# Performance work log

Measured on AMD Instinct MI355X. Metric: run time of the kernel, lower is better.

The kernel has to match this reference:

```python
import jax, jax.numpy as jnp
import numpy as np


def _conv(x, w, b, stride, pad):
    # x: [N,C,H,W], w: [O,I,kh,kw]
    y = jax.lax.conv_general_dilated(
        x, w, (stride, stride), [(pad, pad), (pad, pad)],
        dimension_numbers=('NCHW', 'OIHW', 'NCHW'))
    return y + b[None, :, None, None]


def _block(x, w1, b1, w2, b2, stride):
    # BasicBlock with BN folded: conv3x3 -> relu -> conv3x3
    h = jax.nn.relu(_conv(x, w1, b1, stride, 1))
    return _conv(h, w2, b2, 1, 1)


def setup_inputs() -> dict:
    key = jax.random.key(0)
    keys = iter(jax.random.split(key, 64))

    def rn(shape):
        fan_in = int(np.prod(shape[1:])) if len(shape) > 1 else shape[0]
        return jax.random.normal(next(keys), shape, jnp.float32) * (1.0 / np.sqrt(fan_in))

    d = {}
    d['inputs'] = jax.random.normal(next(keys), (128, 3, 64, 64), jnp.float32)
    d['probs'] = jax.random.uniform(next(keys), (128, 15), jnp.float32)
    d['seed_w'] = rn((64, 3, 3, 3))
    d['seed_b'] = jnp.zeros((64,), jnp.float32)
    specs = [(64, 64), (64, 128), (128, 256)]  # (cin, cout) per group
    for g, (ci, co) in enumerate(specs):
        d[f'g{g}_ds_w'] = rn((co, ci, 1, 1))
        d[f'g{g}_ds_b'] = jnp.zeros((co,), jnp.float32)
        d[f'g{g}_b0_w1'] = rn((co, ci, 3, 3))
        d[f'g{g}_b0_b1'] = jnp.zeros((co,), jnp.float32)
        d[f'g{g}_b0_w2'] = rn((co, co, 3, 3))
        d[f'g{g}_b0_b2'] = jnp.zeros((co,), jnp.float32)
        d[f'g{g}_r_w1'] = rn((4, co, co, 3, 3))
        d[f'g{g}_r_b1'] = jnp.zeros((4, co), jnp.float32)
        d[f'g{g}_r_w2'] = rn((4, co, co, 3, 3))
        d[f'g{g}_r_b2'] = jnp.zeros((4, co), jnp.float32)
    d['fc_w'] = rn((1000, 256))
    d['fc_b'] = jnp.zeros((1000,), jnp.float32)
    return d


def reference(inputs, probs, seed_w, seed_b,
              g0_ds_w, g0_ds_b, g0_b0_w1, g0_b0_b1, g0_b0_w2, g0_b0_b2,
              g0_r_w1, g0_r_b1, g0_r_w2, g0_r_b2,
              g1_ds_w, g1_ds_b, g1_b0_w1, g1_b0_b1, g1_b0_w2, g1_b0_b2,
              g1_r_w1, g1_r_b1, g1_r_w2, g1_r_b2,
              g2_ds_w, g2_ds_b, g2_b0_w1, g2_b0_b1, g2_b0_w2, g2_b0_b2,
              g2_r_w1, g2_r_b1, g2_r_w2, g2_r_b2,
              fc_w, fc_b):
    # policy[k, n] in {0,1}: hard-threshold of agent probs at 0.5 (forward_real)
    policy = jnp.where(probs < 0.5, 0.0, 1.0).astype(inputs.dtype).T  # [15, B]
    x = jax.nn.relu(_conv(inputs, seed_w, seed_b, 1, 1))
    groups = [
        (g0_ds_w, g0_ds_b, g0_b0_w1, g0_b0_b1, g0_b0_w2, g0_b0_b2, g0_r_w1, g0_r_b1, g0_r_w2, g0_r_b2, 1),
        (g1_ds_w, g1_ds_b, g1_b0_w1, g1_b0_b1, g1_b0_w2, g1_b0_b2, g1_r_w1, g1_r_b1, g1_r_w2, g1_r_b2, 2),
        (g2_ds_w, g2_ds_b, g2_b0_w1, g2_b0_b1, g2_b0_w2, g2_b0_b2, g2_r_w1, g2_r_b1, g2_r_w2, g2_r_b2, 2),
    ]
    idx = 0
    for (ds_w, ds_b, b0_w1, b0_b1, b0_w2, b0_b2, r_w1, r_b1, r_w2, r_b2, s) in groups:
        # first block of the group: strided, with 1x1 downsample residual
        residual = _conv(x, ds_w, ds_b, s, 0)
        fx = _block(x, b0_w1, b0_b1, b0_w2, b0_b2, s)
        m = policy[idx][:, None, None, None]
        idx += 1
        x = m * jax.nn.relu(residual + fx) + (1.0 - m) * residual
        # remaining 4 identity-residual blocks
        for j in range(4):
            residual = x
            fx = _block(x, r_w1[j], r_b1[j], r_w2[j], r_b2[j], 1)
            m = policy[idx][:, None, None, None]
            idx += 1
            x = m * jax.nn.relu(residual + fx) + (1.0 - m) * residual
    pooled = x.mean(axis=(2, 3))  # global average pool [B, 256]
    return pooled @ fc_w.T + fc_b
```

## Files before the change

### kernel.cpp

```cpp
#include <hip/hip_runtime.h>

using bf = unsigned short;
typedef __attribute__((ext_vector_type(8))) short short8v;
typedef __attribute__((ext_vector_type(4))) float f32x4;
typedef __attribute__((ext_vector_type(4))) unsigned int u32x4;
typedef __attribute__((ext_vector_type(2))) unsigned int u32x2;

__device__ __forceinline__ float bf2f(bf u) { return __uint_as_float(((unsigned)u) << 16); }
__device__ __forceinline__ bf f2bf(float f) {
    unsigned x = __float_as_uint(f);
    x += 0x7fffu + ((x >> 16) & 1u);
    return (bf)(x >> 16);
}

__device__ __forceinline__ void gload16(const bf* g, bf* l) {
    __builtin_amdgcn_global_load_lds(
        (const __attribute__((address_space(1))) void*)g,
        (__attribute__((address_space(3))) void*)l, 16, 0, 0);
}

template <int CI, int CC, int RS, int STRIDE, bool RELU, int CMB, int TH, int TW, int W>
__global__ __launch_bounds__(256, 3) void conv_mfma(
    const bf* __restrict__ X, const bf* __restrict__ Wp,
    const float* __restrict__ bias, bf* __restrict__ Y,
    const bf* __restrict__ res, const float* __restrict__ probs,
    const bf* __restrict__ zpage, int kidx, int Co) {
    constexpr int PAD = (RS == 3) ? 1 : 0;
    constexpr int IN_ROWS = (TH - 1) * STRIDE + RS;
    constexpr int IN_COLS = (TW - 1) * STRIDE + RS;
    constexpr int NG = CC / 8;
    constexpr int HIN = W * STRIDE;
    constexpr int RSRS = RS * RS;
    constexpr int NCH = CI / CC;
    constexpr bool DIRECT = (RS == 1);
    constexpr int TG = IN_ROWS * IN_COLS * NG;
    constexpr int NITER = (TG + 255) / 256;
    constexpr int NPX = TH * TW;
    constexpr int NF = NPX / 32;
    constexpr int TPR = W / TW;
    constexpr int KSH = (STRIDE == 2) ? 1 : 0;

    __shared__ bf sX[DIRECT ? 8 : IN_ROWS * IN_COLS * CC];

    const int tid = threadIdx.x;
    const int n = blockIdx.z;
    const int coBase = blockIdx.y << 6;
    const int bx = blockIdx.x;
    const int tr0 = (bx / TPR) * TH;
    const int tc0 = (bx % TPR) * TW;

    bool active = true;
    if (kidx >= 0) active = (probs[n * 15 + kidx] >= 0.5f);
    if (!active) return;

    const int lane = tid & 63;
    const int wid = tid >> 6;
    const int l15 = lane & 15;
    const int lq = lane >> 4;
    const int wm = wid >> 1;
    const int wn = wid & 1;

    f32x4 acc[2][NF] = {};
    int prow[NF], pcol[NF];
#pragma unroll
    for (int nf = 0; nf < NF; ++nf) {
        int p = wn * (NPX / 2) + nf * 16 + l15;
        prow[nf] = p / TW;
        pcol[nf] = p % TW;
    }

    const bf* Xn = X + (size_t)n * HIN * HIN * CI;

    if constexpr (DIRECT) {
#pragma unroll
        for (int ch = 0; ch < NCH; ++ch) {
#pragma unroll
            for (int kk = 0; kk < CC / 32; ++kk) {
                short8v a[2], b[NF];
#pragma unroll
                for (int mf = 0; mf < 2; ++mf) {
                    int co = coBase + wm * 32 + mf * 16 + l15;
                    a[mf] = *reinterpret_cast<const short8v*>(
                        Wp + ((size_t)ch * Co + co) * CC + kk * 32 + lq * 8);
                }
#pragma unroll
                for (int nf = 0; nf < NF; ++nf) {
                    b[nf] = *reinterpret_cast<const short8v*>(
                        Xn + ((size_t)((tr0 + prow[nf]) * STRIDE) * HIN +
                              (tc0 + pcol[nf]) * STRIDE) * CI + ch * CC + kk * 32 + lq * 8);
                }
#pragma unroll
                for (int mf = 0; mf < 2; ++mf)
#pragma unroll
                    for (int nf = 0; nf < NF; ++nf)
                        acc[mf][nf] = __builtin_amdgcn_mfma_f32_16x16x32_bf16(
                            a[mf], b[nf], acc[mf][nf], 0, 0, 0);
            }
        }
    } else {
        for (int ch = 0; ch < NCH; ++ch) {
            if (ch) __syncthreads();
#pragma unroll
            for (int i = 0; i < NITER; ++i) {
                int g = tid + i * 256;
                if (TG % 256 == 0 || g < TG) {
                    int ir = g / (IN_COLS * NG);
                    int rem = g - ir * (IN_COLS * NG);
                    int ic = rem / NG;
                    int gc = rem - ic * NG;
                    int in_r = tr0 * STRIDE - PAD + ir;
                    int in_c = tc0 * STRIDE - PAD + ic;
                    int gsrc = gc ^ ((ic >> KSH) & (NG - 1));
                    const bf* src = zpage;
                    if ((unsigned)in_r < (unsigned)HIN && (unsigned)in_c < (unsigned)HIN)
                        src = Xn + ((size_t)in_r * HIN + in_c) * CI + ch * CC + gsrc * 8;
                    gload16(src, &sX[(size_t)g * 8]);
                }
            }
            __syncthreads();

            if constexpr (CC >= 32) {
#pragma unroll
                for (int j = 0; j < RSRS; ++j) {
                    const int dh = j / RS;
                    const int dw = j % RS;
#pragma unroll
                    for (int kk = 0; kk < CC / 32; ++kk) {
                        short8v a[2], b[NF];
#pragma unroll
                        for (int mf = 0; mf < 2; ++mf) {
                            int co = coBase + wm * 32 + mf * 16 + l15;
                            a[mf] = *reinterpret_cast<const short8v*>(
                                Wp + (((size_t)(ch * RSRS + j) * Co + co) * CC + kk * 32 + lq * 8));
                        }
#pragma unroll
                        for (int nf = 0; nf < NF; ++nf) {
                            int ir = prow[nf] * STRIDE + dh;
                            int ic = pcol[nf] * STRIDE + dw;
                            int gk = (kk * 4 + lq) ^ ((ic >> KSH) & (NG - 1));
                            b[nf] = *reinterpret_cast<const short8v*>(
                                &sX[((ir * IN_COLS + ic) * NG + gk) * 8]);
                        }
#pragma unroll
                        for (int mf = 0; mf < 2; ++mf)
#pragma unroll
                            for (int nf = 0; nf < NF; ++nf)
                                acc[mf][nf] = __builtin_amdgcn_mfma_f32_16x16x32_bf16(
                                    a[mf], b[nf], acc[mf][nf], 0, 0, 0);
                    }
                }
            } else {
#pragma unroll
                for (int kt = 0; kt < 3; ++kt) {
                    int j = kt * 4 + lq;
                    int jj = (j < 9) ? j : 0;
                    int dh = jj / 3, dw = jj % 3;
                    short8v a[2], b[NF];
#pragma unroll
                    for (int mf = 0; mf < 2; ++mf) {
                        int co = coBase + wm * 32 + mf * 16 + l15;
                        a[mf] = *reinterpret_cast<const short8v*>(Wp + ((size_t)j * Co + co) * 8);
                    }
#pragma unroll
                    for (int nf = 0; nf < NF; ++nf) {
                        int ir = prow[nf] + dh;
                        int ic = pcol[nf] + dw;
                        b[nf] = *reinterpret_cast<const short8v*>(&sX[(ir * IN_COLS + ic) * 8]);
                    }
#pragma unroll
                    for (int mf = 0; mf < 2; ++mf)
#pragma unroll
                        for (int nf = 0; nf < NF; ++nf)
                            acc[mf][nf] = __builtin_amdgcn_mfma_f32_16x16x32_bf16(
                                a[mf], b[nf], acc[mf][nf], 0, 0, 0);
                }
            }
        }
    }

#pragma unroll
    for (int mf = 0; mf < 2; ++mf) {
        int co0 = coBase + wm * 32 + mf * 16 + lq * 4;
        float4 b4 = *reinterpret_cast<const float4*>(bias + co0);
        float bb[4] = {b4.x, b4.y, b4.z, b4.w};
#pragma unroll
        for (int nf = 0; nf < NF; ++nf) {
            size_t off = ((size_t)n * W * W + (size_t)(tr0 + prow[nf]) * W + tc0 + pcol[nf]) * Co + co0;
            float v[4];
#pragma unroll
            for (int i = 0; i < 4; ++i) v[i] = acc[mf][nf][i] + bb[i];
            if constexpr (CMB >= 1) {
                u32x2 r2 = *reinterpret_cast<const u32x2*>(res + off);
                bf rr[4] = {(bf)(r2[0] & 0xffff), (bf)(r2[0] >> 16),
                            (bf)(r2[1] & 0xffff), (bf)(r2[1] >> 16)};
#pragma unroll
                for (int i = 0; i < 4; ++i) v[i] = fmaxf(v[i] + bf2f(rr[i]), 0.f);
            }
            if constexpr (RELU) {
#pragma unroll
                for (int i = 0; i < 4; ++i) v[i] = fmaxf(v[i], 0.f);
            }
            unsigned lo = (unsigned)f2bf(v[0]) | ((unsigned)f2bf(v[1]) << 16);
            unsigned hi = (unsigned)f2bf(v[2]) | ((unsigned)f2bf(v[3]) << 16);
            u32x2 o2 = {lo, hi};
            *reinterpret_cast<u32x2*>(Y + off) = o2;
        }
    }
}

#define NSEG 34
struct Seg {
    const float* src;
    bf* dst;
    int Co, Ci, RSRS, CC, JPAD, blk0;
};
struct SegArgs {
    Seg s[NSEG];
};
__global__ void repack_all(SegArgs A) {
    int b = blockIdx.x;
    int lo = 0;
#pragma unroll 1
    for (int i = 1; i < NSEG; ++i)
        if (A.s[i].blk0 <= b) lo = i;
    Seg sg = A.s[lo];
    int NCH_ = (sg.Ci + sg.CC - 1) / sg.CC;
    size_t total8 = ((size_t)NCH_ * sg.JPAD * sg.Co * sg.CC) >> 3;
    size_t i8 = (size_t)(b - sg.blk0) * 256 + threadIdx.x;
    if (i8 >= total8) return;
    size_t e = i8 * 8;
    int cw = (int)(e % sg.CC);
    int co = (int)((e / sg.CC) % sg.Co);
    int j = (int)((e / ((size_t)sg.CC * sg.Co)) % sg.JPAD);
    int ch = (int)(e / ((size_t)sg.CC * sg.Co * sg.JPAD));
    bf tmp[8];
#pragma unroll
    for (int k = 0; k < 8; ++k) {
        int ci = ch * sg.CC + cw + k;
        float v = 0.f;
        if (ci < sg.Ci && j < sg.RSRS) v = sg.src[((size_t)co * sg.Ci + ci) * sg.RSRS + j];
        tmp[k] = f2bf(v);
    }
    u32x4 o;
#pragma unroll
    for (int k = 0; k < 4; ++k) o[k] = (unsigned)tmp[2 * k] | ((unsigned)tmp[2 * k + 1] << 16);
    *reinterpret_cast<u32x4*>(sg.dst + e) = o;
}

__global__ void cvt_in(const float* __restrict__ in, bf* __restrict__ out) {
    size_t idx = (size_t)blockIdx.x * 256 + threadIdx.x;
    int c = (int)(idx & 7);
    size_t pix = idx >> 3;
    int w = (int)(pix & 63);
    int h = (int)((pix >> 6) & 63);
    int n = (int)(pix >> 12);
    float v = 0.f;
    if (c < 3) v = in[(((size_t)n * 3 + c) * 64 + h) * 64 + w];
    out[idx] = f2bf(v);
}

__global__ void zero_k(bf* p) {
    u32x4 z = {0, 0, 0, 0};
    *reinterpret_cast<u32x4*>(p + (size_t)threadIdx.x * 8) = z;
}

__global__ void pool_k(const bf* __restrict__ X, float* __restrict__ pooled) {
    __shared__ float red[8][256];
    int n = blockIdx.x;
    int g = threadIdx.x & 31;
    int slice = threadIdx.x >> 5;
    float acc[8] = {};
    for (int p = slice * 32; p < slice * 32 + 32; ++p) {
        u32x4 v = *reinterpret_cast<const u32x4*>(X + ((size_t)n * 256 + p) * 256 + g * 8);
#pragma unroll
        for (int i = 0; i < 4; ++i) {
            acc[2 * i] += bf2f((bf)(v[i] & 0xffff));
            acc[2 * i + 1] += bf2f((bf)(v[i] >> 16));
        }
    }
#pragma unroll
    for (int i = 0; i < 8; ++i) red[slice][g * 8 + i] = acc[i];
    __syncthreads();
    if (slice == 0) {
#pragma unroll
        for (int i = 0; i < 8; ++i) {
            float s = 0.f;
#pragma unroll
            for (int ss = 0; ss < 8; ++ss) s += red[ss][g * 8 + i];
            pooled[n * 256 + g * 8 + i] = s * (1.f / 256.f);
        }
    }
}

__global__ void fc_k(const float* __restrict__ pooled, const float* __restrict__ fw,
                     const float* __restrict__ fb, float* __restrict__ out) {
    __shared__ float sp[256];
    int n = blockIdx.x;
    sp[threadIdx.x] = pooled[n * 256 + threadIdx.x];
    __syncthreads();
    for (int o = threadIdx.x; o < 1000; o += 256) {
        float acc = fb[o];
        for (int k = 0; k < 256; ++k) acc += sp[k] * fw[(size_t)o * 256 + k];
        out[(size_t)n * 1000 + o] = acc;
    }
}

template <int CIN, int COUT, int S, int TH, int TW, int W, int CC1>
static void run_group(hipStream_t st, bf* X, bf* H, bf* OUT, const bf* zp,
                      bf* wp_ds, const float* ds_b, bf* wp_w1, const float* b1,
                      bf* wp_w2, const float* b2, bf* const* wp_rw1, const float* rb1,
                      bf* const* wp_rw2, const float* rb2, const float* probs_c,
                      int kbase, int NB) {
    dim3 grid((W / TH) * (W / TW), COUT / 64, NB);
    conv_mfma<CIN, 64, 1, S, false, 0, TH, TW, W><<<grid, 256, 0, st>>>(
        X, wp_ds, ds_b, OUT, nullptr, nullptr, zp, -1, COUT);
    conv_mfma<CIN, CC1, 3, S, true, 0, TH, TW, W><<<grid, 256, 0, st>>>(
        X, wp_w1, b1, H, nullptr, probs_c, zp, kbase, COUT);
    conv_mfma<COUT, 64, 3, 1, false, 2, TH, TW, W><<<grid, 256, 0, st>>>(
        H, wp_w2, b2, OUT, OUT, probs_c, zp, kbase, COUT);
    for (int j = 0; j < 4; ++j) {
        conv_mfma<COUT, 64, 3, 1, true, 0, TH, TW, W><<<grid, 256, 0, st>>>(
            OUT, wp_rw1[j], rb1 + j * COUT, H, nullptr, probs_c, zp, kbase + 1 + j, COUT);
        conv_mfma<COUT, 64, 3, 1, false, 2, TH, TW, W><<<grid, 256, 0, st>>>(
            H, wp_rw2[j], rb2 + j * COUT, OUT, OUT, probs_c, zp, kbase + 1 + j, COUT);
    }
}

extern "C" void kernel_launch(void* const* d_in, const int* in_sizes, int n_in,
                              void* d_out, int out_size, void* d_ws, size_t ws_size,
                              hipStream_t stream) {
    (void)in_sizes; (void)n_in; (void)out_size;
    const float* input = (const float*)d_in[0];
    const float* probs = (const float*)d_in[1];
    const float* seed_w = (const float*)d_in[2];
    const float* seed_b = (const float*)d_in[3];
    const float* fc_w = (const float*)d_in[34];
    const float* fc_b = (const float*)d_in[35];

    char* pw = (char*)d_ws;
    auto alloc = [&](size_t bytes) -> void* {
        void* r = (void*)pw;
        pw += ((bytes + 255) & ~(size_t)255);
        return r;
    };

    bf* xin = (bf*)alloc(128ull * 64 * 64 * 8 * 2);
    float* pooled = (float*)alloc(128 * 256 * 4);
    bf* zpage = (bf*)alloc(256);

    SegArgs sa;
    int nseg = 0;
    int blkAcc = 0;
    auto pack = [&](const float* w, int Co_, int Ci_, int RSRS_, int CC_, int JPAD_) -> bf* {
        int NCH_ = (Ci_ + CC_ - 1) / CC_;
        size_t total = (size_t)NCH_ * JPAD_ * Co_ * CC_;
        bf* wp = (bf*)alloc(total * 2);
        sa.s[nseg] = {w, wp, Co_, Ci_, RSRS_, CC_, JPAD_, blkAcc};
        blkAcc += (int)(((total >> 3) + 255) / 256);
        ++nseg;
        return wp;
    };

    zero_k<<<dim3(1), 16, 0, stream>>>(zpage);
    cvt_in<<<dim3(16384), 256, 0, stream>>>(input, xin);

    bf* wpSeed = pack(seed_w, 64, 3, 9, 8, 12);
    const int cis[3] = {64, 64, 128};
    const int cos[3] = {64, 128, 256};
    const int cc1s[3] = {64, 32, 32};
    bf* wp_ds[3];
    bf* wp_w1[3];
    bf* wp_w2[3];
    bf* wp_rw1[3][4];
    bf* wp_rw2[3][4];
    const float *ds_b[3], *b1[3], *b2[3], *rb1[3], *rb2[3];
    for (int g = 0; g < 3; ++g) {
        int base = 4 + g * 10;
        const float* dsw = (const float*)d_in[base + 0];
        ds_b[g] = (const float*)d_in[base + 1];
        const float* w1 = (const float*)d_in[base + 2];
        b1[g] = (const float*)d_in[base + 3];
        const float* w2 = (const float*)d_in[base + 4];
        b2[g] = (const float*)d_in[base + 5];
        const float* rw1 = (const float*)d_in[base + 6];
        rb1[g] = (const float*)d_in[base + 7];
        const float* rw2 = (const float*)d_in[base + 8];
        rb2[g] = (const float*)d_in[base + 9];
        int Ci = cis[g], Co = cos[g];
        wp_ds[g] = pack(dsw, Co, Ci, 1, 64, 1);
        wp_w1[g] = pack(w1, Co, Ci, 9, cc1s[g], 9);
        wp_w2[g] = pack(w2, Co, Co, 9, 64, 9);
        for (int j = 0; j < 4; ++j) {
            wp_rw1[g][j] = pack(rw1 + (size_t)j * Co * Co * 9, Co, Co, 9, 64, 9);
            wp_rw2[g][j] = pack(rw2 + (size_t)j * Co * Co * 9, Co, Co, 9, 64, 9);
        }
    }
    for (int i = nseg; i < NSEG; ++i) sa.s[i] = {nullptr, nullptr, 1, 1, 1, 1, 1, 0x7fffffff};
    repack_all<<<dim3(blkAcc), 256, 0, stream>>>(sa);

    size_t used = (size_t)(pw - (char*)d_ws);
    size_t avail = (ws_size > used) ? (ws_size - used) : 0;
    const size_t PER_IMG = 64ull * 64 * 64 * 2;
    int NB = 128;
    while (NB > 8 && (size_t)3 * NB * PER_IMG + 4096 > avail) NB >>= 1;

    bf* A = (bf*)alloc((size_t)NB * PER_IMG);
    bf* Bb = (bf*)alloc((size_t)NB * PER_IMG);
    bf* C = (bf*)alloc((size_t)NB * PER_IMG);

    for (int n0 = 0; n0 < 128; n0 += NB) {
        const float* pc = probs + (size_t)n0 * 15;
        conv_mfma<8, 8, 3, 1, true, 0, 8, 16, 64><<<dim3(32, 1, NB), 256, 0, stream>>>(
            xin + (size_t)n0 * 64 * 64 * 8, wpSeed, seed_b, A, nullptr, nullptr, zpage, -1, 64);

        run_group<64, 64, 1, 8, 16, 64, 64>(stream, A, Bb, C, zpage,
                                            wp_ds[0], ds_b[0], wp_w1[0], b1[0],
                                            wp_w2[0], b2[0], wp_rw1[0], rb1[0],
                                            wp_rw2[0], rb2[0], pc, 0, NB);
        run_group<64, 128, 2, 8, 16, 32, 32>(stream, C, Bb, A, zpage,
                                             wp_ds[1], ds_b[1], wp_w1[1], b1[1],
                                             wp_w2[1], b2[1], wp_rw1[1], rb1[1],
                                             wp_rw2[1], rb2[1], pc, 5, NB);
        run_group<128, 256, 2, 8, 8, 16, 32>(stream, A, Bb, C, zpage,
                                             wp_ds[2], ds_b[2], wp_w1[2], b1[2],
                                             wp_w2[2], b2[2], wp_rw1[2], rb1[2],
                                             wp_rw2[2], rb2[2], pc, 10, NB);

        pool_k<<<dim3(NB), 256, 0, stream>>>(C, pooled + (size_t)n0 * 256);
    }

    fc_k<<<dim3(128), 256, 0, stream>>>(pooled, fc_w, fc_b, (float*)d_out);
}
```

Before: 2.360 ms.

## Double-buffer conv input tiles and fuse input conversion, zeroing and pool+fc

Adds double-buffered LDS staging to the conv kernel when there are multiple channel chunks and two buffers fit in shared memory. The next chunk's global-to-LDS loads can then be issued while MFMAs run on the current chunk, and one barrier per chunk is removed. The seed conv now reads the fp32 NCHW input directly and converts it in-kernel, which drops the separate cvt_in pass. Zero-page init is folded into repack_all and pool+fc are merged into one kernel. The extra LDS use in double-buffered configs may lower occupancy.

```diff
diff --git a/kernel.cpp b/kernel.cpp
--- a/kernel.cpp
+++ b/kernel.cpp
@@ -19,12 +19,14 @@
         (__attribute__((address_space(3))) void*)l, 16, 0, 0);
 }
 
-template <int CI, int CC, int RS, int STRIDE, bool RELU, int CMB, int TH, int TW, int W>
+template <int CI, int CC, int RS, int STRIDE, bool SEED, bool RELU, int CMB,
+          int TH, int TW, int W>
 __global__ __launch_bounds__(256, 3) void conv_mfma(
-    const bf* __restrict__ X, const bf* __restrict__ Wp,
-    const float* __restrict__ bias, bf* __restrict__ Y,
-    const bf* __restrict__ res, const float* __restrict__ probs,
-    const bf* __restrict__ zpage, int kidx, int Co) {
+    const bf* __restrict__ X, const float* __restrict__ Xf,
+    const bf* __restrict__ Wp, const float* __restrict__ bias,
+    bf* __restrict__ Y, const bf* __restrict__ res,
+    const float* __restrict__ probs, const bf* __restrict__ zpage,
+    int kidx, int Co) {
     constexpr int PAD = (RS == 3) ? 1 : 0;
     constexpr int IN_ROWS = (TH - 1) * STRIDE + RS;
     constexpr int IN_COLS = (TW - 1) * STRIDE + RS;
@@ -39,8 +41,10 @@
     constexpr int NF = NPX / 32;
     constexpr int TPR = W / TW;
     constexpr int KSH = (STRIDE == 2) ? 1 : 0;
-
-    __shared__ bf sX[DIRECT ? 8 : IN_ROWS * IN_COLS * CC];
+    constexpr int HALF = IN_ROWS * IN_COLS * CC;
+    constexpr bool DBUF = (!DIRECT) && (!SEED) && (NCH > 1) && (2 * HALF * 2 <= 65536);
+
+    __shared__ bf sX[DIRECT ? 8 : (DBUF ? 2 * HALF : HALF)];
 
     const int tid = threadIdx.x;
     const int n = blockIdx.z;
@@ -98,27 +102,44 @@
             }
         }
     } else {
-        for (int ch = 0; ch < NCH; ++ch) {
-            if (ch) __syncthreads();
-#pragma unroll
-            for (int i = 0; i < NITER; ++i) {
-                int g = tid + i * 256;
-                if (TG % 256 == 0 || g < TG) {
-                    int ir = g / (IN_COLS * NG);
-                    int rem = g - ir * (IN_COLS * NG);
-                    int ic = rem / NG;
-                    int gc = rem - ic * NG;
-                    int in_r = tr0 * STRIDE - PAD + ir;
-                    int in_c = tc0 * STRIDE - PAD + ic;
-                    int gsrc = gc ^ ((ic >> KSH) & (NG - 1));
-                    const bf* src = zpage;
-                    if ((unsigned)in_r < (unsigned)HIN && (unsigned)in_c < (unsigned)HIN)
-                        src = Xn + ((size_t)in_r * HIN + in_c) * CI + ch * CC + gsrc * 8;
-                    gload16(src, &sX[(size_t)g * 8]);
-                }
-            }
-            __syncthreads();
-
+        auto stage = [&](int ch, bf* buf) {
+            if constexpr (SEED) {
+                const float* Xfn = Xf + (size_t)n * 3 * HIN * HIN;
+                if (tid < TG) {
+                    int ir = tid / IN_COLS;
+                    int ic = tid % IN_COLS;
+                    int in_r = tr0 - PAD + ir;
+                    int in_c = tc0 - PAD + ic;
+                    u32x4 u = {0, 0, 0, 0};
+                    if ((unsigned)in_r < (unsigned)HIN && (unsigned)in_c < (unsigned)HIN) {
+                        const float* p = Xfn + (size_t)in_r * HIN + in_c;
+                        u[0] = (unsigned)f2bf(p[0]) | ((unsigned)f2bf(p[HIN * HIN]) << 16);
+                        u[1] = (unsigned)f2bf(p[2 * HIN * HIN]);
+                    }
+                    *reinterpret_cast<u32x4*>(&buf[(size_t)tid * 8]) = u;
+                }
+            } else {
+#pragma unroll
+                for (int i = 0; i < NITER; ++i) {
+                    int g = tid + i * 256;
+                    if (TG % 256 == 0 || g < TG) {
+                        int ir = g / (IN_COLS * NG);
+                        int rem = g - ir * (IN_COLS * NG);
+                        int ic = rem / NG;
+                        int gc = rem - ic * NG;
+                        int in_r = tr0 * STRIDE - PAD + ir;
+                        int in_c = tc0 * STRIDE - PAD + ic;
+                        int gsrc = gc ^ ((ic >> KSH) & (NG - 1));
+                        const bf* src = zpage;
+                        if ((unsigned)in_r < (unsigned)HIN && (unsigned)in_c < (unsigned)HIN)
+                            src = Xn + ((size_t)in_r * HIN + in_c) * CI + ch * CC + gsrc * 8;
+                        gload16(src, &buf[(size_t)g * 8]);
+                    }
+                }
+            }
+        };
+
+        auto compute = [&](int ch, const bf* buf) {
             if constexpr (CC >= 32) {
 #pragma unroll
                 for (int j = 0; j < RSRS; ++j) {
@@ -139,7 +160,7 @@
                             int ic = pcol[nf] * STRIDE + dw;
                             int gk = (kk * 4 + lq) ^ ((ic >> KSH) & (NG - 1));
                             b[nf] = *reinterpret_cast<const short8v*>(
-                                &sX[((ir * IN_COLS + ic) * NG + gk) * 8]);
+                                &buf[((ir * IN_COLS + ic) * NG + gk) * 8]);
                         }
 #pragma unroll
                         for (int mf = 0; mf < 2; ++mf)
@@ -165,7 +186,7 @@
                     for (int nf = 0; nf < NF; ++nf) {
                         int ir = prow[nf] + dh;
                         int ic = pcol[nf] + dw;
-                        b[nf] = *reinterpret_cast<const short8v*>(&sX[(ir * IN_COLS + ic) * 8]);
+                        b[nf] = *reinterpret_cast<const short8v*>(&buf[(ir * IN_COLS + ic) * 8]);
                     }
 #pragma unroll
                     for (int mf = 0; mf < 2; ++mf)
@@ -174,6 +195,26 @@
                             acc[mf][nf] = __builtin_amdgcn_mfma_f32_16x16x32_bf16(
                                 a[mf], b[nf], acc[mf][nf], 0, 0, 0);
                 }
+            }
+        };
+
+        if constexpr (DBUF) {
+            stage(0, sX);
+            __syncthreads();
+#pragma unroll
+            for (int ch = 0; ch < NCH; ++ch) {
+                bf* cur = sX + (size_t)(ch & 1) * HALF;
+                bf* nxt = sX + (size_t)((ch + 1) & 1) * HALF;
+                if (ch + 1 < NCH) stage(ch + 1, nxt);
+                compute(ch, cur);
+                if (ch + 1 < NCH) __syncthreads();
+            }
+        } else {
+            for (int ch = 0; ch < NCH; ++ch) {
+                if (ch) __syncthreads();
+                stage(ch, sX);
+                __syncthreads();
+                compute(ch, sX);
             }
         }
     }
@@ -216,9 +257,14 @@
 };
 struct SegArgs {
     Seg s[NSEG];
+    bf* zpage;
 };
 __global__ void repack_all(SegArgs A) {
     int b = blockIdx.x;
+    if (b == 0 && threadIdx.x < 16) {
+        u32x4 z = {0, 0, 0, 0};
+        *reinterpret_cast<u32x4*>(A.zpage + (size_t)threadIdx.x * 8) = z;
+    }
     int lo = 0;
 #pragma unroll 1
     for (int i = 1; i < NSEG; ++i)
@@ -247,25 +293,10 @@
     *reinterpret_cast<u32x4*>(sg.dst + e) = o;
 }
 
-__global__ void cvt_in(const float* __restrict__ in, bf* __restrict__ out) {
-    size_t idx = (size_t)blockIdx.x * 256 + threadIdx.x;
-    int c = (int)(idx & 7);
-    size_t pix = idx >> 3;
-    int w = (int)(pix & 63);
-    int h = (int)((pix >> 6) & 63);
-    int n = (int)(pix >> 12);
-    float v = 0.f;
-    if (c < 3) v = in[(((size_t)n * 3 + c) * 64 + h) * 64 + w];
-    out[idx] = f2bf(v);
-}
-
-__global__ void zero_k(bf* p) {
-    u32x4 z = {0, 0, 0, 0};
-    *reinterpret_cast<u32x4*>(p + (size_t)threadIdx.x * 8) = z;
-}
-
-__global__ void pool_k(const bf* __restrict__ X, float* __restrict__ pooled) {
+__global__ void poolfc_k(const bf* __restrict__ X, const float* __restrict__ fw,
+                         const float* __restrict__ fb, float* __restrict__ out) {
     __shared__ float red[8][256];
+    __shared__ float sp[256];
     int n = blockIdx.x;
     int g = threadIdx.x & 31;
     int slice = threadIdx.x >> 5;
@@ -287,21 +318,14 @@
             float s = 0.f;
 #pragma unroll
             for (int ss = 0; ss < 8; ++ss) s += red[ss][g * 8 + i];
-            pooled[n * 256 + g * 8 + i] = s * (1.f / 256.f);
-        }
-    }
-}
-
-__global__ void fc_k(const float* __restrict__ pooled, const float* __restrict__ fw,
-                     const float* __restrict__ fb, float* __restrict__ out) {
-    __shared__ float sp[256];
-    int n = blockIdx.x;
-    sp[threadIdx.x] = pooled[n * 256 + threadIdx.x];
+            sp[g * 8 + i] = s * (1.f / 256.f);
+        }
+    }
     __syncthreads();
     for (int o = threadIdx.x; o < 1000; o += 256) {
-        float acc = fb[o];
-        for (int k = 0; k < 256; ++k) acc += sp[k] * fw[(size_t)o * 256 + k];
-        out[(size_t)n * 1000 + o] = acc;
+        float a = fb[o];
+        for (int k = 0; k < 256; ++k) a += sp[k] * fw[(size_t)o * 256 + k];
+        out[(size_t)n * 1000 + o] = a;
     }
 }
 
@@ -312,17 +336,19 @@
                       bf* const* wp_rw2, const float* rb2, const float* probs_c,
                       int kbase, int NB) {
     dim3 grid((W / TH) * (W / TW), COUT / 64, NB);
-    conv_mfma<CIN, 64, 1, S, false, 0, TH, TW, W><<<grid, 256, 0, st>>>(
-        X, wp_ds, ds_b, OUT, nullptr, nullptr, zp, -1, COUT);
-    conv_mfma<CIN, CC1, 3, S, true, 0, TH, TW, W><<<grid, 256, 0, st>>>(
-        X, wp_w1, b1, H, nullptr, probs_c, zp, kbase, COUT);
-    conv_mfma<COUT, 64, 3, 1, false, 2, TH, TW, W><<<grid, 256, 0, st>>>(
-        H, wp_w2, b2, OUT, OUT, probs_c, zp, kbase, COUT);
+    conv_mfma<CIN, 64, 1, S, false, false, 0, TH, TW, W><<<grid, 256, 0, st>>>(
+        X, nullptr, wp_ds, ds_b, OUT, nullptr, nullptr, zp, -1, COUT);
+    conv_mfma<CIN, CC1, 3, S, false, true, 0, TH, TW, W><<<grid, 256, 0, st>>>(
+        X, nullptr, wp_w1, b1, H, nullptr, probs_c, zp, kbase, COUT);
+    conv_mfma<COUT, 64, 3, 1, false, false, 2, TH, TW, W><<<grid, 256, 0, st>>>(
+        H, nullptr, wp_w2, b2, OUT, OUT, probs_c, zp, kbase, COUT);
     for (int j = 0; j < 4; ++j) {
-        conv_mfma<COUT, 64, 3, 1, true, 0, TH, TW, W><<<grid, 256, 0, st>>>(
-            OUT, wp_rw1[j], rb1 + j * COUT, H, nullptr, probs_c, zp, kbase + 1 + j, COUT);
-        conv_mfma<COUT, 64, 3, 1, false, 2, TH, TW, W><<<grid, 256, 0, st>>>(
-            H, wp_rw2[j], rb2 + j * COUT, OUT, OUT, probs_c, zp, kbase + 1 + j, COUT);
+        conv_mfma<COUT, 64, 3, 1, false, true, 0, TH, TW, W><<<grid, 256, 0, st>>>(
+            OUT, nullptr, wp_rw1[j], rb1 + j * COUT, H, nullptr, probs_c, zp,
+            kbase + 1 + j, COUT);
+        conv_mfma<COUT, 64, 3, 1, false, false, 2, TH, TW, W><<<grid, 256, 0, st>>>(
+            H, nullptr, wp_rw2[j], rb2 + j * COUT, OUT, OUT, probs_c, zp,
+            kbase + 1 + j, COUT);
     }
 }
 
@@ -344,11 +370,10 @@
         return r;
     };
 
-    bf* xin = (bf*)alloc(128ull * 64 * 64 * 8 * 2);
-    float* pooled = (float*)alloc(128 * 256 * 4);
     bf* zpage = (bf*)alloc(256);
 
     SegArgs sa;
+    sa.zpage = zpage;
     int nseg = 0;
     int blkAcc = 0;
     auto pack = [&](const float* w, int Co_, int Ci_, int RSRS_, int CC_, int JPAD_) -> bf* {
@@ -360,9 +385,6 @@
         ++nseg;
         return wp;
     };
-
-    zero_k<<<dim3(1), 16, 0, stream>>>(zpage);
-    cvt_in<<<dim3(16384), 256, 0, stream>>>(input, xin);
 
     bf* wpSeed = pack(seed_w, 64, 3, 9, 8, 12);
     const int cis[3] = {64, 64, 128};
@@ -410,8 +432,9 @@
 
     for (int n0 = 0; n0 < 128; n0 += NB) {
         const float* pc = probs + (size_t)n0 * 15;
-        conv_mfma<8, 8, 3, 1, true, 0, 8, 16, 64><<<dim3(32, 1, NB), 256, 0, stream>>>(
-            xin + (size_t)n0 * 64 * 64 * 8, wpSeed, seed_b, A, nullptr, nullptr, zpage, -1, 64);
+        conv_mfma<8, 8, 3, 1, true, true, 0, 8, 16, 64><<<dim3(32, 1, NB), 256, 0, stream>>>(
+            nullptr, input + (size_t)n0 * 3 * 4096, wpSeed, seed_b, A, nullptr,
+            nullptr, zpage, -1, 64);
 
         run_group<64, 64, 1, 8, 16, 64, 64>(stream, A, Bb, C, zpage,
                                             wp_ds[0], ds_b[0], wp_w1[0], b1[0],
@@ -426,8 +449,7 @@
                                              wp_w2[2], b2[2], wp_rw1[2], rb1[2],
                                              wp_rw2[2], rb2[2], pc, 10, NB);
 
-        pool_k<<<dim3(NB), 256, 0, stream>>>(C, pooled + (size_t)n0 * 256);
-    }
-
-    fc_k<<<dim3(128), 256, 0, stream>>>(pooled, fc_w, fc_b, (float*)d_out);
-}
+        poolfc_k<<<dim3(NB), 256, 0, stream>>>(C, fc_w, fc_b,
+                                               (float*)d_out + (size_t)n0 * 1000);
+    }
+}
```

After: 2.217 ms. 6.1% less time.
